# Performance work log

Measured on AMD Instinct MI355X. Metric: run time of the kernel, lower is better.

Reference implementation:

```python
import jax, jax.numpy as jnp
import numpy as np

NU, NI, K, D, B = 100000, 50000, 100, 64, 8192


def setup_inputs() -> dict:
    key = jax.random.key(0)
    ks = jax.random.split(key, 16)
    s = lambda fan_in: np.sqrt(2.0 / fan_in)  # kaiming_normal-ish scale
    return {
        "user_emb": jax.random.normal(ks[0], (NU, D), jnp.float32) * s(D),
        "item_emb": jax.random.normal(ks[1], (NI, D), jnp.float32) * s(D),
        "user_scr_tensor": jax.random.uniform(ks[2], (NU, K), jnp.float32) / K,
        "item_scr_tensor": jax.random.uniform(ks[3], (NI, K), jnp.float32) / K,
        "w1": jax.random.normal(ks[4], (64, 128), jnp.float32) * s(128),
        "b1": jnp.zeros((64,), jnp.float32),
        "w2": jax.random.normal(ks[5], (64, 64), jnp.float32) * s(64),
        "b2": jnp.zeros((64,), jnp.float32),
        "w3": jax.random.normal(ks[6], (32, 64), jnp.float32) * s(64),
        "b3": jnp.zeros((32,), jnp.float32),
        "w4": jax.random.normal(ks[7], (32, 32), jnp.float32) * s(32),
        "b4": jnp.zeros((32,), jnp.float32),
        "w5": jax.random.normal(ks[8], (1, 32), jnp.float32) * s(32),
        "b5": jnp.zeros((1,), jnp.float32),
        "user_idx_tensor": jax.random.randint(ks[9], (NU, K), 0, NU, jnp.int32),
        "item_idx_tensor": jax.random.randint(ks[10], (NI, K), 0, NI, jnp.int32),
        "user_idxs": jax.random.randint(ks[11], (B,), 0, NU, jnp.int32),
        "item_idxs": jax.random.randint(ks[12], (B,), 0, NI, jnp.int32),
    }


def _scored_pool(idx_tensor, emb, scr, idxs):
    neighs = idx_tensor[idxs]          # [B, K]
    neigh_emb = emb[neighs]            # [B, K, D]
    neigh_scr = scr[neighs]            # [B, K, K]
    return jnp.einsum("bkj,bjd->bkd", neigh_scr, neigh_emb)


def reference(user_emb, item_emb, user_scr_tensor, item_scr_tensor,
              w1, b1, w2, b2, w3, b3, w4, b4, w5, b5,
              user_idx_tensor, item_idx_tensor, user_idxs, item_idxs):
    su = _scored_pool(user_idx_tensor, user_emb, user_scr_tensor, user_idxs)  # [B,K,D]
    si = _scored_pool(item_idx_tensor, item_emb, item_scr_tensor, item_idxs)  # [B,K,D]
    x = jnp.concatenate([su, si], axis=2)  # [B, K, 2D]
    x = jax.nn.relu(x @ w1.T + b1)
    x = jax.nn.relu(x @ w2.T + b2)
    x = jax.nn.relu(x @ w3.T + b3)
    x = jax.nn.relu(x @ w4.T + b4)
    x = jax.nn.sigmoid(x @ w5.T + b5)  # [B, K, 1]
    return jnp.mean(x, axis=-2).squeeze()  # [B]
```

## Files before the change

kernel.cpp:

```cpp
#include <hip/hip_runtime.h>
#include <hip/hip_bf16.h>
#include <math.h>

typedef __attribute__((ext_vector_type(8))) short short8;
typedef __attribute__((ext_vector_type(4))) float f32x4;

#define KN 100

#define W1_OFF 0
#define W2_OFF 8192
#define W3_OFF 12288
#define W4_OFF 14336
#define SCRU_OFF 16384
#define SCRI_OFF (SCRU_OFF + 100000 * 128)
#define EMBU_OFF (SCRI_OFF + 50000 * 128)
#define EMBI_OFF (EMBU_OFF + 100000 * 64)

#define ET_STRIDE 136
#define ET_OFF 14336
#define S_TOT  (14336 + 64 * ET_STRIDE)

__device__ __forceinline__ unsigned short f2bf(float f) {
  __hip_bfloat16 h = __float2bfloat16(f);
  return __builtin_bit_cast(unsigned short, h);
}

__device__ __forceinline__ void st8(unsigned short* d, float4 a, float4 b) {
  short8 h;
  h[0] = (short)f2bf(a.x); h[1] = (short)f2bf(a.y);
  h[2] = (short)f2bf(a.z); h[3] = (short)f2bf(a.w);
  h[4] = (short)f2bf(b.x); h[5] = (short)f2bf(b.y);
  h[6] = (short)f2bf(b.z); h[7] = (short)f2bf(b.w);
  *reinterpret_cast<short8*>(d) = h;
}

__device__ __forceinline__ short8 pk2(f32x4 a, f32x4 b) {
  short8 h;
  h[0] = (short)f2bf(a[0]); h[1] = (short)f2bf(a[1]);
  h[2] = (short)f2bf(a[2]); h[3] = (short)f2bf(a[3]);
  h[4] = (short)f2bf(b[0]); h[5] = (short)f2bf(b[1]);
  h[6] = (short)f2bf(b[2]); h[7] = (short)f2bf(b[3]);
  return h;
}

#define PREP_UNITS (15360 + 2400000 + 1200000)
__global__ void prep(const float* __restrict__ w1, const float* __restrict__ w2,
                     const float* __restrict__ w3, const float* __restrict__ w4,
                     const float* __restrict__ uscr, const float* __restrict__ iscr,
                     const float* __restrict__ uemb, const float* __restrict__ iemb,
                     unsigned short* __restrict__ ws) {
  const float4 z4 = {0.f, 0.f, 0.f, 0.f};
  const int stride = gridDim.x * 256;
  for (int t = blockIdx.x * 256 + threadIdx.x; t < PREP_UNITS; t += stride) {
    if (t < 15360) {
      const float* src; int rel, o, i, kt, base;
      if (t < 8192)       { src = w1; rel = t;         o = rel >> 7; i = rel & 127; kt = 4; base = W1_OFF; }
      else if (t < 12288) { src = w2; rel = t - 8192;  o = rel >> 6; i = rel & 63;  kt = 2; base = W2_OFF; }
      else if (t < 14336) { src = w3; rel = t - 12288; o = rel >> 6; i = rel & 63;  kt = 2; base = W3_OFF; }
      else                { src = w4; rel = t - 14336; o = rel >> 5; i = rel & 31;  kt = 1; base = W4_OFF; }
      int n = o >> 4, l15 = o & 15, k = i >> 5;
      int quad = (i >> 2) & 3, s = ((i >> 4) & 1) * 4 + (i & 3);
      ws[base + ((n * kt + k) * 64 + quad * 16 + l15) * 8 + s] = f2bf(src[rel]);
      continue;
    }
    int rel = t - 15360;
    if (rel < 2400000) {
      const float* src; unsigned short* dst; int row, g;
      if (rel < 1600000) {
        row = rel >> 4; g = rel & 15;
        src = uscr + (size_t)row * 100;
        dst = ws + SCRU_OFF + (size_t)row * 128 + g * 8;
      } else {
        int q = rel - 1600000; row = q >> 4; g = q & 15;
        src = iscr + (size_t)row * 100;
        dst = ws + SCRI_OFF + (size_t)row * 128 + g * 8;
      }
      const int jb = 32 * (g >> 2) + 4 * (g & 3);
      float4 va = (jb <= 96) ? *reinterpret_cast<const float4*>(src + jb) : z4;
      float4 vb = (jb <= 80) ? *reinterpret_cast<const float4*>(src + jb + 16) : z4;
      st8(dst, va, vb);
      continue;
    }
    rel -= 2400000;
    {
      const float* src; unsigned short* dst; int row, g;
      if (rel < 800000) {
        row = rel >> 3; g = rel & 7;
        src = uemb + (size_t)row * 64;
        dst = ws + EMBU_OFF + (size_t)row * 64 + g * 8;
      } else {
        int q = rel - 800000; row = q >> 3; g = q & 7;
        src = iemb + (size_t)row * 64;
        dst = ws + EMBI_OFF + (size_t)row * 64 + g * 8;
      }
      float4 va = *reinterpret_cast<const float4*>(src + g * 8);
      float4 vb = *reinterpret_cast<const float4*>(src + g * 8 + 4);
      st8(dst, va, vb);
    }
  }
}

__device__ __forceinline__ void pool_mfma(const unsigned short* __restrict__ Sb,
                                          const short8* sb, int l15, int quad,
                                          short8& f0, short8& f1) {
  f32x4 acc[4];
#pragma unroll
  for (int po = 0; po < 4; ++po) acc[po] = (f32x4){0.f, 0.f, 0.f, 0.f};
#pragma unroll
  for (int k4 = 0; k4 < 4; ++k4) {
#pragma unroll
    for (int po = 0; po < 4; ++po) {
      const int row = po * 16 + l15;
      const int hw = row * ET_STRIDE + (((k4 * 4 + quad) ^ ((row >> 3) & 7)) << 3);
      short8 ea = *reinterpret_cast<const short8*>(Sb + hw);
      acc[po] = __builtin_amdgcn_mfma_f32_16x16x32_bf16(ea, sb[k4], acc[po], 0, 0, 0);
    }
  }
  f0 = pk2(acc[0], acc[1]);
  f1 = pk2(acc[2], acc[3]);
}

__device__ __forceinline__ void et_store(unsigned short* __restrict__ S,
                                         const unsigned int* ev, int w, int c,
                                         int half) {
#pragma unroll
  for (int rr = 0; rr < 8; ++rr) {
    const int rbase = w + rr * 7;
    if (rbase < 50) {
      const int r0 = rbase * 2;
      const int p0 = ((r0 >> 5) << 5) | (((r0 >> 2) & 3) << 3) |
                     (((r0 >> 4) & 1) << 2) | (r0 & 3);
      const int sw = ((c >> 2) & 7) << 3;
      const int q = (2 * c + half) * ET_STRIDE + (p0 ^ sw);
      unsigned int v = ev[rr];
      unsigned int p = __shfl_xor(v, 32, 64);
      unsigned int d = half ? ((v & 0xffff0000u) | (p >> 16))
                            : ((v & 0x0000ffffu) | (p << 16));
      *reinterpret_cast<unsigned int*>(&S[ET_OFF + q]) = d;
    }
  }
}

__launch_bounds__(448, 5)
__global__ void cnn_mfma8(
    const unsigned short* __restrict__ ws,
    const float* __restrict__ b1, const float* __restrict__ b2,
    const float* __restrict__ b3, const float* __restrict__ b4,
    const float* __restrict__ w5, const float* __restrict__ b5,
    const int* __restrict__ user_idx_t, const int* __restrict__ item_idx_t,
    const int* __restrict__ user_idxs, const int* __restrict__ item_idxs,
    float* __restrict__ out) {
  __shared__ __align__(16) unsigned short S[S_TOT];
  __shared__ int s_nb[2][112];
  __shared__ float s_red[7];

  const int b = blockIdx.x;
  const int tid = threadIdx.x;
  const int w = tid >> 6;
  const int lane = tid & 63;
  const int l15 = lane & 15, quad = lane >> 4;

  short8 wtmp[4];
#pragma unroll
  for (int i = 0; i < 4; ++i)
    wtmp[i] = reinterpret_cast<const short8*>(ws)[tid + i * 448];

  if (tid < 112) {
    s_nb[0][tid] = (tid < KN) ? user_idx_t[(size_t)user_idxs[b] * KN + tid] : 0;
  } else if (tid >= 128 && tid < 240) {
    int i = tid - 128;
    s_nb[1][i] = (i < KN) ? item_idx_t[(size_t)item_idxs[b] * KN + i] : 0;
  }

  {
    const short8 z8 = {0, 0, 0, 0, 0, 0, 0, 0};
    if (tid < 256) {
      const int row = tid >> 2, ci = tid & 3;
      const int chunk = (12 + ci) ^ ((row >> 3) & 7);
      *reinterpret_cast<short8*>(&S[ET_OFF + row * ET_STRIDE + chunk * 8]) = z8;
    }
  }

#pragma unroll
  for (int i = 0; i < 4; ++i)
    reinterpret_cast<short8*>(S)[tid + i * 448] = wtmp[i];
  __syncthreads();

  const int mrow = w * 16 + l15;
  const int c = lane & 31, half = lane >> 5;
  const int* nbu = s_nb[0];
  const int* nbi = s_nb[1];

  unsigned int evu[8], evi[8];
#pragma unroll
  for (int rr = 0; rr < 8; ++rr) {
    const int rbase = w + rr * 7;
    if (rbase < 50) {
      const int r = rbase * 2 + half;
      evu[rr] = *reinterpret_cast<const unsigned int*>(
          ws + EMBU_OFF + (size_t)nbu[r] * 64 + c * 2);
      evi[rr] = *reinterpret_cast<const unsigned int*>(
          ws + EMBI_OFF + (size_t)nbi[r] * 64 + c * 2);
    } else {
      evu[rr] = 0u; evi[rr] = 0u;
    }
  }
  short8 sbu[4], sbi[4];
  {
    const unsigned short* arow = ws + SCRU_OFF + (size_t)nbu[mrow] * 128;
#pragma unroll
    for (int k = 0; k < 4; ++k)
      sbu[k] = *reinterpret_cast<const short8*>(arow + k * 32 + quad * 8);
  }
  {
    const unsigned short* arow = ws + SCRI_OFF + (size_t)nbi[mrow] * 128;
#pragma unroll
    for (int k = 0; k < 4; ++k)
      sbi[k] = *reinterpret_cast<const short8*>(arow + k * 32 + quad * 8);
  }

  et_store(S, evu, w, c, half);
  __syncthreads();
  short8 x0, x1, x2, x3;
  pool_mfma(S + ET_OFF, sbu, l15, quad, x0, x1);
  __syncthreads();

  et_store(S, evi, w, c, half);
  __syncthreads();
  pool_mfma(S + ET_OFF, sbi, l15, quad, x2, x3);

  f32x4 y[4];
#pragma unroll
  for (int po = 0; po < 4; ++po) y[po] = (f32x4){0.f, 0.f, 0.f, 0.f};
  {
    short8 xf[4] = {x0, x1, x2, x3};
#pragma unroll
    for (int k4 = 0; k4 < 4; ++k4)
#pragma unroll
      for (int po = 0; po < 4; ++po) {
        short8 wa = *reinterpret_cast<const short8*>(
            S + W1_OFF + ((po * 4 + k4) * 64 + lane) * 8);
        y[po] = __builtin_amdgcn_mfma_f32_16x16x32_bf16(wa, xf[k4], y[po], 0, 0, 0);
      }
  }
#pragma unroll
  for (int po = 0; po < 4; ++po) {
    const float4 bb = *reinterpret_cast<const float4*>(b1 + po * 16 + quad * 4);
#pragma unroll
    for (int r = 0; r < 4; ++r) y[po][r] = fmaxf(y[po][r] + bb[r], 0.f);
  }
  short8 g0 = pk2(y[0], y[1]), g1 = pk2(y[2], y[3]);

  f32x4 v[4];
#pragma unroll
  for (int po = 0; po < 4; ++po) v[po] = (f32x4){0.f, 0.f, 0.f, 0.f};
#pragma unroll
  for (int k4 = 0; k4 < 2; ++k4) {
    short8 gf = k4 ? g1 : g0;
#pragma unroll
    for (int po = 0; po < 4; ++po) {
      short8 wa = *reinterpret_cast<const short8*>(
          S + W2_OFF + ((po * 2 + k4) * 64 + lane) * 8);
      v[po] = __builtin_amdgcn_mfma_f32_16x16x32_bf16(wa, gf, v[po], 0, 0, 0);
    }
  }
#pragma unroll
  for (int po = 0; po < 4; ++po) {
    const float4 bb = *reinterpret_cast<const float4*>(b2 + po * 16 + quad * 4);
#pragma unroll
    for (int r = 0; r < 4; ++r) v[po][r] = fmaxf(v[po][r] + bb[r], 0.f);
  }
  short8 h0 = pk2(v[0], v[1]), h1 = pk2(v[2], v[3]);

  f32x4 t3[2];
  t3[0] = (f32x4){0.f, 0.f, 0.f, 0.f};
  t3[1] = (f32x4){0.f, 0.f, 0.f, 0.f};
#pragma unroll
  for (int k4 = 0; k4 < 2; ++k4) {
    short8 gf = k4 ? h1 : h0;
#pragma unroll
    for (int po = 0; po < 2; ++po) {
      short8 wa = *reinterpret_cast<const short8*>(
          S + W3_OFF + ((po * 2 + k4) * 64 + lane) * 8);
      t3[po] = __builtin_amdgcn_mfma_f32_16x16x32_bf16(wa, gf, t3[po], 0, 0, 0);
    }
  }
#pragma unroll
  for (int po = 0; po < 2; ++po) {
    const float4 bb = *reinterpret_cast<const float4*>(b3 + po * 16 + quad * 4);
#pragma unroll
    for (int r = 0; r < 4; ++r) t3[po][r] = fmaxf(t3[po][r] + bb[r], 0.f);
  }
  short8 q0 = pk2(t3[0], t3[1]);

  f32x4 u[2];
  u[0] = (f32x4){0.f, 0.f, 0.f, 0.f};
  u[1] = (f32x4){0.f, 0.f, 0.f, 0.f};
#pragma unroll
  for (int po = 0; po < 2; ++po) {
    short8 wa = *reinterpret_cast<const short8*>(ws + W4_OFF + (po * 64 + lane) * 8);
    u[po] = __builtin_amdgcn_mfma_f32_16x16x32_bf16(wa, q0, u[po], 0, 0, 0);
  }
  float part = 0.f;
#pragma unroll
  for (int po = 0; po < 2; ++po) {
    const float4 bb = *reinterpret_cast<const float4*>(b4 + po * 16 + quad * 4);
    const float4 wv = *reinterpret_cast<const float4*>(w5 + po * 16 + quad * 4);
#pragma unroll
    for (int r = 0; r < 4; ++r)
      part = fmaf(fmaxf(u[po][r] + bb[r], 0.f), wv[r], part);
  }
  part += __shfl_xor(part, 16, 64);
  part += __shfl_xor(part, 32, 64);
  float sig = 1.f / (1.f + expf(-(part + b5[0])));
  if (mrow >= KN) sig = 0.f;
  sig += __shfl_xor(sig, 1, 64);
  sig += __shfl_xor(sig, 2, 64);
  sig += __shfl_xor(sig, 4, 64);
  sig += __shfl_xor(sig, 8, 64);
  if (lane == 0) s_red[w] = sig;
  __syncthreads();
  if (tid == 0) {
    float acc = 0.f;
#pragma unroll
    for (int i = 0; i < 7; ++i) acc += s_red[i];
    out[b] = acc * (1.0f / KN);
  }
}

extern "C" void kernel_launch(void* const* d_in, const int* in_sizes, int n_in,
                              void* d_out, int out_size, void* d_ws,
                              size_t ws_size, hipStream_t stream) {
  const float* user_emb = (const float*)d_in[0];
  const float* item_emb = (const float*)d_in[1];
  const float* user_scr = (const float*)d_in[2];
  const float* item_scr = (const float*)d_in[3];
  const float* w1 = (const float*)d_in[4];
  const float* b1 = (const float*)d_in[5];
  const float* w2 = (const float*)d_in[6];
  const float* b2 = (const float*)d_in[7];
  const float* w3 = (const float*)d_in[8];
  const float* b3 = (const float*)d_in[9];
  const float* w4 = (const float*)d_in[10];
  const float* b4 = (const float*)d_in[11];
  const float* w5 = (const float*)d_in[12];
  const float* b5 = (const float*)d_in[13];
  const int* user_idx_t = (const int*)d_in[14];
  const int* item_idx_t = (const int*)d_in[15];
  const int* user_idxs = (const int*)d_in[16];
  const int* item_idxs = (const int*)d_in[17];
  unsigned short* wsw = (unsigned short*)d_ws;

  prep<<<dim3(2048), dim3(256), 0, stream>>>(
      w1, w2, w3, w4, user_scr, item_scr, user_emb, item_emb, wsw);

  const int B = in_sizes[16];
  cnn_mfma8<<<dim3(B), dim3(448), 0, stream>>>(
      wsw, b1, b2, b3, b4, w5, b5, user_idx_t, item_idx_t, user_idxs,
      item_idxs, (float*)d_out);
}
```

Baseline: 351.2 us.

## Double-buffer embedding tiles, load neighbor indices into registers, and cut barriers

Gives the user and item embedding tiles separate LDS buffers, so both are stored before a single barrier and the two pooling MFMAs run back to back. This removes three of the four __syncthreads. Neighbor indices now go straight from global memory into registers instead of being staged in shared memory, which drops one barrier-dependent round trip. The larger LDS footprint lowers the launch bound from 5 to 4 blocks per CU, which may reduce occupancy.

```diff
diff --git a/kernel.cpp b/kernel.cpp
--- a/kernel.cpp
+++ b/kernel.cpp
@@ -17,8 +17,9 @@
 #define EMBI_OFF (EMBU_OFF + 100000 * 64)
 
 #define ET_STRIDE 136
-#define ET_OFF 14336
-#define S_TOT  (14336 + 64 * ET_STRIDE)
+#define ETU_OFF 14336
+#define ETI_OFF (14336 + 64 * ET_STRIDE)
+#define S_TOT   (14336 + 2 * 64 * ET_STRIDE)
 
 __device__ __forceinline__ unsigned short f2bf(float f) {
   __hip_bfloat16 h = __float2bfloat16(f);
@@ -122,7 +123,7 @@
 
 __device__ __forceinline__ void et_store(unsigned short* __restrict__ S,
                                          const unsigned int* ev, int w, int c,
-                                         int half) {
+                                         int half, int base) {
 #pragma unroll
   for (int rr = 0; rr < 8; ++rr) {
     const int rbase = w + rr * 7;
@@ -136,13 +137,13 @@
       unsigned int p = __shfl_xor(v, 32, 64);
       unsigned int d = half ? ((v & 0xffff0000u) | (p >> 16))
                             : ((v & 0x0000ffffu) | (p << 16));
-      *reinterpret_cast<unsigned int*>(&S[ET_OFF + q]) = d;
-    }
-  }
-}
-
-__launch_bounds__(448, 5)
-__global__ void cnn_mfma8(
+      *reinterpret_cast<unsigned int*>(&S[base + q]) = d;
+    }
+  }
+}
+
+__launch_bounds__(448, 4)
+__global__ void cnn_mfma9(
     const unsigned short* __restrict__ ws,
     const float* __restrict__ b1, const float* __restrict__ b2,
     const float* __restrict__ b3, const float* __restrict__ b4,
@@ -151,7 +152,6 @@
     const int* __restrict__ user_idxs, const int* __restrict__ item_idxs,
     float* __restrict__ out) {
   __shared__ __align__(16) unsigned short S[S_TOT];
-  __shared__ int s_nb[2][112];
   __shared__ float s_red[7];
 
   const int b = blockIdx.x;
@@ -159,75 +159,86 @@
   const int w = tid >> 6;
   const int lane = tid & 63;
   const int l15 = lane & 15, quad = lane >> 4;
+  const int mrow = w * 16 + l15;
+  const int c = lane & 31, half = lane >> 5;
 
   short8 wtmp[4];
 #pragma unroll
   for (int i = 0; i < 4; ++i)
     wtmp[i] = reinterpret_cast<const short8*>(ws)[tid + i * 448];
 
-  if (tid < 112) {
-    s_nb[0][tid] = (tid < KN) ? user_idx_t[(size_t)user_idxs[b] * KN + tid] : 0;
-  } else if (tid >= 128 && tid < 240) {
-    int i = tid - 128;
-    s_nb[1][i] = (i < KN) ? item_idx_t[(size_t)item_idxs[b] * KN + i] : 0;
-  }
-
-  {
-    const short8 z8 = {0, 0, 0, 0, 0, 0, 0, 0};
-    if (tid < 256) {
-      const int row = tid >> 2, ci = tid & 3;
-      const int chunk = (12 + ci) ^ ((row >> 3) & 7);
-      *reinterpret_cast<short8*>(&S[ET_OFF + row * ET_STRIDE + chunk * 8]) = z8;
-    }
-  }
-
-#pragma unroll
-  for (int i = 0; i < 4; ++i)
-    reinterpret_cast<short8*>(S)[tid + i * 448] = wtmp[i];
-  __syncthreads();
-
-  const int mrow = w * 16 + l15;
-  const int c = lane & 31, half = lane >> 5;
-  const int* nbu = s_nb[0];
-  const int* nbi = s_nb[1];
-
-  unsigned int evu[8], evi[8];
+  const int ub = user_idxs[b] * KN;
+  const int ibx = item_idxs[b] * KN;
+  int nbu_s[8], nbi_s[8];
 #pragma unroll
   for (int rr = 0; rr < 8; ++rr) {
     const int rbase = w + rr * 7;
     if (rbase < 50) {
       const int r = rbase * 2 + half;
+      nbu_s[rr] = user_idx_t[ub + r];
+      nbi_s[rr] = item_idx_t[ibx + r];
+    } else {
+      nbu_s[rr] = 0; nbi_s[rr] = 0;
+    }
+  }
+  const int mr = (mrow < KN) ? mrow : 0;
+  const int nbu_m = user_idx_t[ub + mr];
+  const int nbi_m = item_idx_t[ibx + mr];
+
+  unsigned int evu[8], evi[8];
+#pragma unroll
+  for (int rr = 0; rr < 8; ++rr) {
+    const int rbase = w + rr * 7;
+    if (rbase < 50) {
       evu[rr] = *reinterpret_cast<const unsigned int*>(
-          ws + EMBU_OFF + (size_t)nbu[r] * 64 + c * 2);
+          ws + EMBU_OFF + (size_t)nbu_s[rr] * 64 + c * 2);
       evi[rr] = *reinterpret_cast<const unsigned int*>(
-          ws + EMBI_OFF + (size_t)nbi[r] * 64 + c * 2);
+          ws + EMBI_OFF + (size_t)nbi_s[rr] * 64 + c * 2);
     } else {
       evu[rr] = 0u; evi[rr] = 0u;
     }
   }
   short8 sbu[4], sbi[4];
   {
-    const unsigned short* arow = ws + SCRU_OFF + (size_t)nbu[mrow] * 128;
+    const unsigned short* arow = ws + SCRU_OFF + (size_t)nbu_m * 128;
 #pragma unroll
     for (int k = 0; k < 4; ++k)
       sbu[k] = *reinterpret_cast<const short8*>(arow + k * 32 + quad * 8);
   }
   {
-    const unsigned short* arow = ws + SCRI_OFF + (size_t)nbi[mrow] * 128;
+    const unsigned short* arow = ws + SCRI_OFF + (size_t)nbi_m * 128;
 #pragma unroll
     for (int k = 0; k < 4; ++k)
       sbi[k] = *reinterpret_cast<const short8*>(arow + k * 32 + quad * 8);
   }
 
-  et_store(S, evu, w, c, half);
+  {
+    const short8 z8 = {0, 0, 0, 0, 0, 0, 0, 0};
+    const uint2 z2 = {0u, 0u};
+    for (int i = tid; i < 512; i += 448) {
+      const int buf = i >> 8;
+      const int rem = i & 255;
+      const int row = rem >> 2, ci = rem & 3;
+      const int sw = (row >> 3) & 7;
+      const int base = (buf ? ETI_OFF : ETU_OFF) + row * ET_STRIDE;
+      if (ci == 0) {
+        *reinterpret_cast<uint2*>(&S[base + ((12 ^ sw) << 3) + 4]) = z2;
+      } else {
+        *reinterpret_cast<short8*>(&S[base + (((12 + ci) ^ sw) << 3)]) = z8;
+      }
+    }
+  }
+
+#pragma unroll
+  for (int i = 0; i < 4; ++i)
+    reinterpret_cast<short8*>(S)[tid + i * 448] = wtmp[i];
+  et_store(S, evu, w, c, half, ETU_OFF);
+  et_store(S, evi, w, c, half, ETI_OFF);
   __syncthreads();
+
   short8 x0, x1, x2, x3;
-  pool_mfma(S + ET_OFF, sbu, l15, quad, x0, x1);
-  __syncthreads();
-
-  et_store(S, evi, w, c, half);
-  __syncthreads();
-  pool_mfma(S + ET_OFF, sbi, l15, quad, x2, x3);
+  pool_mfma(S + ETU_OFF, sbu, l15, quad, x0, x1);
+  pool_mfma(S + ETI_OFF, sbi, l15, quad, x2, x3);
 
   f32x4 y[4];
 #pragma unroll
@@ -355,7 +366,7 @@
       w1, w2, w3, w4, user_scr, item_scr, user_emb, item_emb, wsw);
 
   const int B = in_sizes[16];
-  cnn_mfma8<<<dim3(B), dim3(448), 0, stream>>>(
+  cnn_mfma9<<<dim3(B), dim3(448), 0, stream>>>(
       wsw, b1, b2, b3, b4, w5, b5, user_idx_t, item_idx_t, user_idxs,
       item_idxs, (float*)d_out);
 }
```

After: 353.7 us. No clear change (+0.7%).
